# Kernel optimization log

Measured on AMD Instinct MI355X. Metric: run time of the kernel, lower is better.

## Reference

```python
import jax, jax.numpy as jnp
import numpy as np

B, T, F = 16384, 48, 4
UNITS = 256
OUT_STEPS = 24


def setup_inputs() -> dict:
    key = jax.random.key(0)
    ks = jax.random.split(key, 6)
    s_x = 1.0 / np.sqrt(F)
    s_h = 1.0 / np.sqrt(UNITS)
    return {
        "x": jax.random.normal(ks[0], (B, T, F), jnp.float32),
        "Wx": jax.random.normal(ks[1], (F, 4 * UNITS), jnp.float32) * s_x,
        "Wh": jax.random.normal(ks[2], (UNITS, 4 * UNITS), jnp.float32) * s_h,
        "b": jnp.zeros((4 * UNITS,), jnp.float32),
        "Wd": jax.random.normal(ks[3], (UNITS, F), jnp.float32) * s_h,
        "bd": jnp.zeros((F,), jnp.float32),
    }


def _lstm_cell(xt, h, c, Wx, Wh, b):
    # Keras LSTMCell gate order: i, f, g(cell candidate), o
    z = xt @ Wx + h @ Wh + b  # [B, 4*units]
    i, f, g, o = jnp.split(z, 4, axis=-1)
    i = jax.nn.sigmoid(i)
    f = jax.nn.sigmoid(f)
    g = jnp.tanh(g)
    o = jax.nn.sigmoid(o)
    c_new = f * c + i * g
    h_new = o * jnp.tanh(c_new)
    return h_new, c_new


def reference(x, Wx, Wh, b, Wd, bd):
    bsz = x.shape[0]
    h0 = jnp.zeros((bsz, UNITS), x.dtype)
    c0 = jnp.zeros((bsz, UNITS), x.dtype)

    # --- warmup: run LSTM over the input window, keep final state ---
    def warm_step(carry, xt):
        h, c = carry
        h, c = _lstm_cell(xt, h, c, Wx, Wh, b)
        return (h, c), None

    (h, c), _ = jax.lax.scan(warm_step, (h0, c0), jnp.swapaxes(x, 0, 1))
    pred0 = h @ Wd + bd  # first prediction [B, F]

    def ar_step(carry, _):
        h, c, pred = carry
        h, c = _lstm_cell(pred, h, c, Wx, Wh, b)
        pred = h @ Wd + bd
        return (h, c, pred), pred

    _, preds = jax.lax.scan(ar_step, (h, c, pred0), None, length=OUT_STEPS - 1)
    preds = jnp.concatenate([pred0[None], preds], axis=0)  # [out_steps, B, F]
    return jnp.swapaxes(preds, 0, 1)  # [B, out_steps, F]
```

## Files before the change

kernel.cpp:

```cpp
#include <hip/hip_runtime.h>


typedef unsigned short u16;
typedef __attribute__((ext_vector_type(8))) short bf16x8;
typedef __attribute__((ext_vector_type(4))) float f32x4;
typedef __attribute__((ext_vector_type(16))) float f32x16;

#define PITCH 296
#define HB 18944
#define WARM 48
#define STEPS 71
#define LOG2E  1.442695041f
#define LOG2E2 2.885390082f

__device__ __forceinline__ u16 f2bf(float f) {
    unsigned u = __float_as_uint(f);
    u += 0x7FFFu + ((u >> 16) & 1u);
    return (u16)(u >> 16);
}

__device__ __forceinline__ unsigned pk_bf16(float a, float b) {
    unsigned d;
    asm("v_cvt_pk_bf16_f32 %0, %1, %2" : "=v"(d) : "v"(a), "v"(b));
    return d;
}

__device__ __forceinline__ void sync_lds() {
    asm volatile("s_waitcnt lgkmcnt(0)\n\ts_barrier" ::: "memory");
}

__global__ void prep_weights(const float* __restrict__ Wx,
                             const float* __restrict__ Wh,
                             const float* __restrict__ b,
                             const float* __restrict__ Wd,
                             const float* __restrict__ bd,
                             u16* __restrict__ whext,
                             u16* __restrict__ wdp) {
    int idx = blockIdx.x * 256 + threadIdx.x;
    if (idx < 34816) {
        int lane = idx & 63;
        int fr = idx >> 6;
        int g = fr & 3;
        int wv = (fr >> 2) & 7;
        int kt = fr >> 5;
        int k0 = kt * 16 + (lane >> 5) * 8;
        int n = 256 * g + 32 * wv + (lane & 31);
        float sc = (g == 2) ? LOG2E2 : LOG2E;
        u16 v[8];
#pragma unroll
        for (int j = 0; j < 8; ++j) {
            int k = k0 + j;
            float f = 0.0f;
            if (k < 256) f = Wh[k * 1024 + n];
            else if (k < 260) f = Wx[(k - 256) * 1024 + n];
            else if (k == 260) f = b[n];
            v[j] = f2bf(f * sc);
        }
        ushort4* dst = (ushort4*)(whext + (size_t)idx * 8);
        dst[0] = make_ushort4(v[0], v[1], v[2], v[3]);
        dst[1] = make_ushort4(v[4], v[5], v[6], v[7]);
    } else if (idx < 34816 + 576) {
        int id2 = idx - 34816;
        int lane = id2 & 63;
        int kc = id2 >> 6;
        int m = lane & 15;
        int k0 = kc * 32 + (lane >> 4) * 8;
        u16 v[8];
#pragma unroll
        for (int j = 0; j < 8; ++j) {
            int k = k0 + j;
            float f = 0.0f;
            if (m < 4) {
                if (k < 256) f = Wd[k * 4 + m];
                else if (k == 260) f = bd[m];
            }
            v[j] = f2bf(f);
        }
        ushort4* dst = (ushort4*)(wdp + (size_t)id2 * 8);
        dst[0] = make_ushort4(v[0], v[1], v[2], v[3]);
        dst[1] = make_ushort4(v[4], v[5], v[6], v[7]);
    }
}

#define WL(DST, T) do {                                                       \
    const char* _p = wpw + ((size_t)(T) << 15);                               \
    DST[0] = *(const bf16x8*)(_p + voffl);                                    \
    DST[1] = *(const bf16x8*)(_p + voffl + 1024);                             \
    DST[2] = *(const bf16x8*)(_p + voffl + 2048);                             \
    DST[3] = *(const bf16x8*)(_p + voffl + 3072);                             \
} while (0)

#define HL(DST, T) do {                                                       \
    DST[0] = *(const bf16x8*)&hr[hrow0 + (T) * 16];                           \
    DST[1] = *(const bf16x8*)&hr[hrow1 + (T) * 16];                           \
} while (0)

#define MT(WA, HBX)                                                           \
    _Pragma("unroll") for (int m = 0; m < 2; ++m)                             \
    _Pragma("unroll") for (int g = 0; g < 4; ++g)                             \
        acc[m][g] = __builtin_amdgcn_mfma_f32_32x32x16_bf16(                  \
            WA[g], HBX[m], acc[m][g], 0, 0, 0);

#define STG(K, AW, HBX) do { MT(AW, HBX); WL(AW, (K) + 3); HL(HBX, (K) + 2); } while (0)

__global__ __launch_bounds__(512, 2) void lstm_main(
    const float* __restrict__ x, const u16* __restrict__ whext,
    const u16* __restrict__ wdp, float* __restrict__ out) {
    __shared__ __align__(16) u16 hbuf[2 * HB];

    const int tid = threadIdx.x;
    const int w = tid >> 6;
    const int l = tid & 63;
    const int l31 = l & 31;
    const int lh = l >> 5;
    const long long rowBase = (long long)blockIdx.x * 64;

    {
        int4 z = make_int4(0, 0, 0, 0);
        for (int i = tid; i < 4736; i += 512) ((int4*)hbuf)[i] = z;
    }
    sync_lds();
    if (tid < 64) {
        hbuf[tid * PITCH + 260] = (u16)0x3F80;
        hbuf[HB + tid * PITCH + 260] = (u16)0x3F80;
        const float4 xv = *(const float4*)(x + (rowBase + tid) * 192);
        uint2* p = (uint2*)&hbuf[tid * PITCH + 256];
        *p = make_uint2(pk_bf16(xv.x, xv.y), pk_bf16(xv.z, xv.w));
    }

    const char* __restrict__ wpw = (const char*)whext + (size_t)w * 4096;
    const char* __restrict__ dp = (const char*)wdp;
    const int voffl = l * 16;
    const int hrow0 = l31 * PITCH + lh * 8;
    const int hrow1 = (32 + l31) * PITCH + lh * 8;

    f32x16 c[2] = {};
    bf16x8 aw0[4], aw1[4], aw2[4];
    WL(aw0, 0);
    WL(aw1, 1);
    WL(aw2, 2);

    for (int step = 0; step < STEPS; ++step) {
        const u16* hr = hbuf + (step & 1) * HB;
        u16* hw = hbuf + ((step & 1) ^ 1) * HB;

        float4 xv = make_float4(0.f, 0.f, 0.f, 0.f);
        if (w == 0 && step < WARM - 1)
            xv = *(const float4*)(x + (rowBase + l) * 192 + (step + 1) * 4);

        sync_lds();

        f32x16 acc[2][4] = {};
        bf16x8 hb0[2], hb1[2];
        HL(hb0, 0);
        HL(hb1, 1);

        STG(0, aw0, hb0);
        STG(1, aw1, hb1);
#pragma unroll 1
        for (int k = 2; k < 14; k += 6) {
            STG(k + 0, aw2, hb0);
            STG(k + 1, aw0, hb1);
            STG(k + 2, aw1, hb0);
            STG(k + 3, aw2, hb1);
            STG(k + 4, aw0, hb0);
            STG(k + 5, aw1, hb1);
        }
        MT(aw2, hb0); WL(aw2, 2); HL(hb0, 16);
        MT(aw0, hb1); WL(aw0, 0);
        MT(aw1, hb0); WL(aw1, 1);

#pragma unroll
        for (int m = 0; m < 2; ++m) {
            const int hwrow = (32 * m + l31) * PITCH + 32 * w + 4 * lh;
#pragma unroll
            for (int q = 0; q < 4; ++q) {
                unsigned pk[2];
#pragma unroll
                for (int hp = 0; hp < 2; ++hp) {
                    float h2[2];
#pragma unroll
                    for (int rr = 0; rr < 2; ++rr) {
                        const int r = q * 4 + hp * 2 + rr;
                        float ei = __builtin_amdgcn_exp2f(-acc[m][0][r]);
                        float ef = __builtin_amdgcn_exp2f(-acc[m][1][r]);
                        float eg = __builtin_amdgcn_exp2f(-acc[m][2][r]);
                        float eo = __builtin_amdgcn_exp2f(-acc[m][3][r]);
                        float ai = 1.0f + ei, af = 1.0f + ef;
                        float ag = 1.0f + eg, ao = 1.0f + eo;
                        float P  = ai * ag;
                        float rD = __builtin_amdgcn_rcpf(P * af);
                        float cn = fmaf(c[m][r] * P, rD, (1.0f - eg) * af * rD);
                        c[m][r] = cn;
                        float ec = __builtin_amdgcn_exp2f(-LOG2E2 * cn);
                        float rE = __builtin_amdgcn_rcpf(ao * (1.0f + ec));
                        h2[rr] = (1.0f - ec) * rE;
                    }
                    pk[hp] = pk_bf16(h2[0], h2[1]);
                }
                *(uint2*)&hw[hwrow + 8 * q] = make_uint2(pk[0], pk[1]);
            }
        }

        if (step < WARM - 1) {
            if (w == 0) {
                uint2* p = (uint2*)&hw[l * PITCH + 256];
                *p = make_uint2(pk_bf16(xv.x, xv.y), pk_bf16(xv.z, xv.w));
            }
        } else {
            sync_lds();
            if (w < 4) {
                f32x4 pacc = {};
                const int col = l & 15;
                const int prow = (16 * w + col) * PITCH + (l >> 4) * 8;
#pragma unroll
                for (int kc = 0; kc < 9; ++kc) {
                    bf16x8 hbp = *(const bf16x8*)&hw[prow + kc * 32];
                    bf16x8 wap = *(const bf16x8*)(dp + ((size_t)kc * 64 + l) * 16);
                    pacc = __builtin_amdgcn_mfma_f32_16x16x32_bf16(wap, hbp, pacc, 0, 0, 0);
                }
                if ((l >> 4) == 0) {
                    int s = step - (WARM - 1);
                    int batch = 16 * w + col;
                    *(float4*)&out[((rowBase + batch) * 24 + s) * 4] =
                        make_float4(pacc[0], pacc[1], pacc[2], pacc[3]);
                    *(uint2*)&hw[batch * PITCH + 256] =
                        make_uint2(pk_bf16(pacc[0], pacc[1]), pk_bf16(pacc[2], pacc[3]));
                }
            }
        }
    }
}

extern "C" void kernel_launch(void* const* d_in, const int* in_sizes, int n_in,
                              void* d_out, int out_size, void* d_ws, size_t ws_size,
                              hipStream_t stream) {
    const float* x  = (const float*)d_in[0];
    const float* Wx = (const float*)d_in[1];
    const float* Wh = (const float*)d_in[2];
    const float* b  = (const float*)d_in[3];
    const float* Wd = (const float*)d_in[4];
    const float* bd = (const float*)d_in[5];
    float* out = (float*)d_out;

    u16* whext = (u16*)d_ws;
    u16* wdp = (u16*)((char*)d_ws + 557056);

    prep_weights<<<(34816 + 576 + 255) / 256, 256, 0, stream>>>(Wx, Wh, b, Wd, bd, whext, wdp);
    lstm_main<<<256, 512, 0, stream>>>(x, whext, wdp, out);
}
```

Before: 744.3 us.

## Halve rows per block to 32 and double grid with higher occupancy

Each block now handles 32 batch rows instead of 64, so the grid doubles to 512 blocks and launch bounds allow 4 blocks per CU. The MFMA tile drops from two M-subtiles to one, and weight prefetch drops from triple buffering to a single buffer reloaded each stage. This aims to raise occupancy and cut per-thread registers and LDS, so more warps hide latency. In exchange, each weight fragment loaded from global/L2 feeds half as many MFMAs, so total weight traffic per batch row doubles and there is less in-flight prefetch.

```diff
diff --git a/kernel.cpp b/kernel.cpp
--- a/kernel.cpp
+++ b/kernel.cpp
@@ -7,7 +7,7 @@
 typedef __attribute__((ext_vector_type(16))) float f32x16;
 
 #define PITCH 296
-#define HB 18944
+#define HB 9472
 #define WARM 48
 #define STEPS 71
 #define LOG2E  1.442695041f
@@ -90,20 +90,16 @@
     DST[3] = *(const bf16x8*)(_p + voffl + 3072);                             \
 } while (0)
 
-#define HL(DST, T) do {                                                       \
-    DST[0] = *(const bf16x8*)&hr[hrow0 + (T) * 16];                           \
-    DST[1] = *(const bf16x8*)&hr[hrow1 + (T) * 16];                           \
-} while (0)
-
-#define MT(WA, HBX)                                                           \
-    _Pragma("unroll") for (int m = 0; m < 2; ++m)                             \
+#define HL1(DST, T) do { DST = *(const bf16x8*)&hr[hrow + (T) * 16]; } while (0)
+
+#define MT1(HBX)                                                              \
     _Pragma("unroll") for (int g = 0; g < 4; ++g)                             \
-        acc[m][g] = __builtin_amdgcn_mfma_f32_32x32x16_bf16(                  \
-            WA[g], HBX[m], acc[m][g], 0, 0, 0);
-
-#define STG(K, AW, HBX) do { MT(AW, HBX); WL(AW, (K) + 3); HL(HBX, (K) + 2); } while (0)
-
-__global__ __launch_bounds__(512, 2) void lstm_main(
+        acc[g] = __builtin_amdgcn_mfma_f32_32x32x16_bf16(                     \
+            aw[g], HBX, acc[g], 0, 0, 0);
+
+#define STG1(K, HBX) do { MT1(HBX); WL(aw, (K) + 1); HL1(HBX, (K) + 2); } while (0)
+
+__global__ __launch_bounds__(512, 4) void lstm_main(
     const float* __restrict__ x, const u16* __restrict__ whext,
     const u16* __restrict__ wdp, float* __restrict__ out) {
     __shared__ __align__(16) u16 hbuf[2 * HB];
@@ -113,14 +109,14 @@
     const int l = tid & 63;
     const int l31 = l & 31;
     const int lh = l >> 5;
-    const long long rowBase = (long long)blockIdx.x * 64;
+    const long long rowBase = (long long)blockIdx.x * 32;
 
     {
         int4 z = make_int4(0, 0, 0, 0);
-        for (int i = tid; i < 4736; i += 512) ((int4*)hbuf)[i] = z;
+        for (int i = tid; i < 2368; i += 512) ((int4*)hbuf)[i] = z;
     }
     sync_lds();
-    if (tid < 64) {
+    if (tid < 32) {
         hbuf[tid * PITCH + 260] = (u16)0x3F80;
         hbuf[HB + tid * PITCH + 260] = (u16)0x3F80;
         const float4 xv = *(const float4*)(x + (rowBase + tid) * 192);
@@ -131,48 +127,38 @@
     const char* __restrict__ wpw = (const char*)whext + (size_t)w * 4096;
     const char* __restrict__ dp = (const char*)wdp;
     const int voffl = l * 16;
-    const int hrow0 = l31 * PITCH + lh * 8;
-    const int hrow1 = (32 + l31) * PITCH + lh * 8;
-
-    f32x16 c[2] = {};
-    bf16x8 aw0[4], aw1[4], aw2[4];
-    WL(aw0, 0);
-    WL(aw1, 1);
-    WL(aw2, 2);
+    const int hrow = l31 * PITCH + lh * 8;
+
+    f32x16 c = {};
+    bf16x8 aw[4];
+    WL(aw, 0);
 
     for (int step = 0; step < STEPS; ++step) {
         const u16* hr = hbuf + (step & 1) * HB;
         u16* hw = hbuf + ((step & 1) ^ 1) * HB;
 
         float4 xv = make_float4(0.f, 0.f, 0.f, 0.f);
-        if (w == 0 && step < WARM - 1)
+        if (w == 0 && l < 32 && step < WARM - 1)
             xv = *(const float4*)(x + (rowBase + l) * 192 + (step + 1) * 4);
 
         sync_lds();
 
-        f32x16 acc[2][4] = {};
-        bf16x8 hb0[2], hb1[2];
-        HL(hb0, 0);
-        HL(hb1, 1);
-
-        STG(0, aw0, hb0);
-        STG(1, aw1, hb1);
+        f32x16 acc[4] = {};
+        bf16x8 hb0, hb1;
+        HL1(hb0, 0);
+        HL1(hb1, 1);
+
 #pragma unroll 1
-        for (int k = 2; k < 14; k += 6) {
-            STG(k + 0, aw2, hb0);
-            STG(k + 1, aw0, hb1);
-            STG(k + 2, aw1, hb0);
-            STG(k + 3, aw2, hb1);
-            STG(k + 4, aw0, hb0);
-            STG(k + 5, aw1, hb1);
-        }
-        MT(aw2, hb0); WL(aw2, 2); HL(hb0, 16);
-        MT(aw0, hb1); WL(aw0, 0);
-        MT(aw1, hb0); WL(aw1, 1);
-
-#pragma unroll
-        for (int m = 0; m < 2; ++m) {
-            const int hwrow = (32 * m + l31) * PITCH + 32 * w + 4 * lh;
+        for (int k = 0; k < 14; k += 2) {
+            STG1(k, hb0);
+            STG1(k + 1, hb1);
+        }
+        MT1(hb0); WL(aw, 15); HL1(hb0, 16);
+        MT1(hb1); WL(aw, 16);
+        MT1(hb0); WL(aw, 0);
+
+        {
+            const int hwrow = l31 * PITCH + 32 * w + 4 * lh;
 #pragma unroll
             for (int q = 0; q < 4; ++q) {
                 unsigned pk[2];
@@ -182,16 +168,16 @@
 #pragma unroll
                     for (int rr = 0; rr < 2; ++rr) {
                         const int r = q * 4 + hp * 2 + rr;
-                        float ei = __builtin_amdgcn_exp2f(-acc[m][0][r]);
-                        float ef = __builtin_amdgcn_exp2f(-acc[m][1][r]);
-                        float eg = __builtin_amdgcn_exp2f(-acc[m][2][r]);
-                        float eo = __builtin_amdgcn_exp2f(-acc[m][3][r]);
+                        float ei = __builtin_amdgcn_exp2f(-acc[0][r]);
+                        float ef = __builtin_amdgcn_exp2f(-acc[1][r]);
+                        float eg = __builtin_amdgcn_exp2f(-acc[2][r]);
+                        float eo = __builtin_amdgcn_exp2f(-acc[3][r]);
                         float ai = 1.0f + ei, af = 1.0f + ef;
                         float ag = 1.0f + eg, ao = 1.0f + eo;
                         float P  = ai * ag;
                         float rD = __builtin_amdgcn_rcpf(P * af);
-                        float cn = fmaf(c[m][r] * P, rD, (1.0f - eg) * af * rD);
-                        c[m][r] = cn;
+                        float cn = fmaf(c[r] * P, rD, (1.0f - eg) * af * rD);
+                        c[r] = cn;
                         float ec = __builtin_amdgcn_exp2f(-LOG2E2 * cn);
                         float rE = __builtin_amdgcn_rcpf(ao * (1.0f + ec));
                         h2[rr] = (1.0f - ec) * rE;
@@ -203,13 +189,13 @@
         }
 
         if (step < WARM - 1) {
-            if (w == 0) {
+            if (w == 0 && l < 32) {
                 uint2* p = (uint2*)&hw[l * PITCH + 256];
                 *p = make_uint2(pk_bf16(xv.x, xv.y), pk_bf16(xv.z, xv.w));
             }
         } else {
             sync_lds();
-            if (w < 4) {
+            if (w < 2) {
                 f32x4 pacc = {};
                 const int col = l & 15;
                 const int prow = (16 * w + col) * PITCH + (l >> 4) * 8;
@@ -247,5 +233,5 @@
     u16* wdp = (u16*)((char*)d_ws + 557056);
 
     prep_weights<<<(34816 + 576 + 255) / 256, 256, 0, stream>>>(Wx, Wh, b, Wd, bd, whext, wdp);
-    lstm_main<<<256, 512, 0, stream>>>(x, whext, wdp, out);
-}
+    lstm_main<<<512, 512, 0, stream>>>(x, whext, wdp, out);
+}
```

Measured after the change: 924.9 us. 24.3% more time.

## Move LSTM cell state to LDS and deepen weight prefetch pipeline

Applied to the files above, without the earlier changes.

The per-thread cell state (32 floats) moves out of registers into a 64KB LDS buffer and is read and written per quad during the gate epilogue. The freed registers hold two more weight fragment buffers, so weight loads are issued five stages ahead instead of three and the K loop is fully unrolled. The goal is to hide global weight-load latency behind MFMA work. In exchange each step adds LDS traffic for the cell state, and total LDS use per block grows a lot, which may limit occupancy at the requested two blocks per CU.

```diff
diff --git a/kernel.cpp b/kernel.cpp
--- a/kernel.cpp
+++ b/kernel.cpp
@@ -101,12 +101,13 @@
         acc[m][g] = __builtin_amdgcn_mfma_f32_32x32x16_bf16(                  \
             WA[g], HBX[m], acc[m][g], 0, 0, 0);
 
-#define STG(K, AW, HBX) do { MT(AW, HBX); WL(AW, (K) + 3); HL(HBX, (K) + 2); } while (0)
+#define STG(K, AW, HBX) do { MT(AW, HBX); WL(AW, (K) + 5); HL(HBX, (K) + 2); } while (0)
 
 __global__ __launch_bounds__(512, 2) void lstm_main(
     const float* __restrict__ x, const u16* __restrict__ whext,
     const u16* __restrict__ wdp, float* __restrict__ out) {
     __shared__ __align__(16) u16 hbuf[2 * HB];
+    __shared__ __align__(16) float cbuf[16384];
 
     const int tid = threadIdx.x;
     const int w = tid >> 6;
@@ -118,6 +119,7 @@
     {
         int4 z = make_int4(0, 0, 0, 0);
         for (int i = tid; i < 4736; i += 512) ((int4*)hbuf)[i] = z;
+        for (int i = tid; i < 4096; i += 512) ((int4*)cbuf)[i] = z;
     }
     sync_lds();
     if (tid < 64) {
@@ -134,11 +136,12 @@
     const int hrow0 = l31 * PITCH + lh * 8;
     const int hrow1 = (32 + l31) * PITCH + lh * 8;
 
-    f32x16 c[2] = {};
-    bf16x8 aw0[4], aw1[4], aw2[4];
+    bf16x8 aw0[4], aw1[4], aw2[4], aw3[4], aw4[4];
     WL(aw0, 0);
     WL(aw1, 1);
     WL(aw2, 2);
+    WL(aw3, 3);
+    WL(aw4, 4);
 
     for (int step = 0; step < STEPS; ++step) {
         const u16* hr = hbuf + (step & 1) * HB;
@@ -157,16 +160,19 @@
 
         STG(0, aw0, hb0);
         STG(1, aw1, hb1);
-#pragma unroll 1
-        for (int k = 2; k < 14; k += 6) {
-            STG(k + 0, aw2, hb0);
-            STG(k + 1, aw0, hb1);
-            STG(k + 2, aw1, hb0);
-            STG(k + 3, aw2, hb1);
-            STG(k + 4, aw0, hb0);
-            STG(k + 5, aw1, hb1);
-        }
-        MT(aw2, hb0); WL(aw2, 2); HL(hb0, 16);
+        STG(2, aw2, hb0);
+        STG(3, aw3, hb1);
+        STG(4, aw4, hb0);
+        STG(5, aw0, hb1);
+        STG(6, aw1, hb0);
+        STG(7, aw2, hb1);
+        STG(8, aw3, hb0);
+        STG(9, aw4, hb1);
+        STG(10, aw0, hb0);
+        STG(11, aw1, hb1);
+        MT(aw2, hb0); WL(aw2, 2); HL(hb0, 14);
+        MT(aw3, hb1); WL(aw3, 3); HL(hb1, 15);
+        MT(aw4, hb0); WL(aw4, 4); HL(hb0, 16);
         MT(aw0, hb1); WL(aw0, 0);
         MT(aw1, hb0); WL(aw1, 1);
 
@@ -175,6 +181,9 @@
             const int hwrow = (32 * m + l31) * PITCH + 32 * w + 4 * lh;
 #pragma unroll
             for (int q = 0; q < 4; ++q) {
+                float* cp = cbuf + ((m * 4 + q) << 11) + (tid << 2);
+                f32x4 cv = *(const f32x4*)cp;
+                f32x4 nv;
                 unsigned pk[2];
 #pragma unroll
                 for (int hp = 0; hp < 2; ++hp) {
@@ -182,6 +191,7 @@
 #pragma unroll
                     for (int rr = 0; rr < 2; ++rr) {
                         const int r = q * 4 + hp * 2 + rr;
+                        const int rc = hp * 2 + rr;
                         float ei = __builtin_amdgcn_exp2f(-acc[m][0][r]);
                         float ef = __builtin_amdgcn_exp2f(-acc[m][1][r]);
                         float eg = __builtin_amdgcn_exp2f(-acc[m][2][r]);
@@ -190,14 +200,15 @@
                         float ag = 1.0f + eg, ao = 1.0f + eo;
                         float P  = ai * ag;
                         float rD = __builtin_amdgcn_rcpf(P * af);
-                        float cn = fmaf(c[m][r] * P, rD, (1.0f - eg) * af * rD);
-                        c[m][r] = cn;
+                        float cn = fmaf(cv[rc] * P, rD, (1.0f - eg) * af * rD);
+                        nv[rc] = cn;
                         float ec = __builtin_amdgcn_exp2f(-LOG2E2 * cn);
                         float rE = __builtin_amdgcn_rcpf(ao * (1.0f + ec));
                         h2[rr] = (1.0f - ec) * rE;
                     }
                     pk[hp] = pk_bf16(h2[0], h2[1]);
                 }
+                *(f32x4*)cp = nv;
                 *(uint2*)&hw[hwrow + 8 * q] = make_uint2(pk[0], pk[1]);
             }
         }
```

Measured after the change: 788.8 us. 6.0% more time.

## Replace per-step block barriers with LDS flag-based producer/consumer sync and triple buffering

Applied to the files above, without the earlier changes.

Removes the workgroup-wide s_barrier at each recurrent step. Each wave now publishes a per-wave LDS flag after writing its slice of h, and consumers spin only on the flags of the h k-tiles they need. The h buffer grows from double to triple buffering so fast waves can run ahead without overwriting data still being read. Each wave also starts its k-loop at a different tile offset, so it can begin on its own freshly written tiles. The cost is spin-polling on volatile LDS loads, more LDS use that may affect occupancy, and a risk of subtle ordering bugs.

```diff
diff --git a/kernel.cpp b/kernel.cpp
--- a/kernel.cpp
+++ b/kernel.cpp
@@ -25,8 +25,25 @@
     return d;
 }
 
-__device__ __forceinline__ void sync_lds() {
-    asm volatile("s_waitcnt lgkmcnt(0)\n\ts_barrier" ::: "memory");
+__device__ __forceinline__ void set_flag(int* f, int v, int lane) {
+    asm volatile("s_waitcnt lgkmcnt(0)" ::: "memory");
+    if (lane == 0) *(volatile int*)f = v;
+}
+
+__device__ __forceinline__ void wait1(const int* f, int tgt) {
+    while (*(volatile const int*)f < tgt) {}
+    asm volatile("" ::: "memory");
+}
+
+__device__ __forceinline__ void wait4(const int* f, int tgt) {
+    for (;;) {
+        int a = ((volatile const int*)f)[0];
+        int b = ((volatile const int*)f)[1];
+        int c = ((volatile const int*)f)[2];
+        int d = ((volatile const int*)f)[3];
+        if (a >= tgt && b >= tgt && c >= tgt && d >= tgt) break;
+    }
+    asm volatile("" ::: "memory");
 }
 
 __global__ void prep_weights(const float* __restrict__ Wx,
@@ -82,17 +99,17 @@
     }
 }
 
-#define WL(DST, T) do {                                                       \
-    const char* _p = wpw + ((size_t)(T) << 15);                               \
+#define WLK(DST, KT) do {                                                     \
+    const char* _p = wpw + ((size_t)(KT) << 15);                              \
     DST[0] = *(const bf16x8*)(_p + voffl);                                    \
     DST[1] = *(const bf16x8*)(_p + voffl + 1024);                             \
     DST[2] = *(const bf16x8*)(_p + voffl + 2048);                             \
     DST[3] = *(const bf16x8*)(_p + voffl + 3072);                             \
 } while (0)
 
-#define HL(DST, T) do {                                                       \
-    DST[0] = *(const bf16x8*)&hr[hrow0 + (T) * 16];                           \
-    DST[1] = *(const bf16x8*)&hr[hrow1 + (T) * 16];                           \
+#define HLD(DST, KT) do {                                                     \
+    DST[0] = *(const bf16x8*)&hr[hrow0 + (KT) * 16];                          \
+    DST[1] = *(const bf16x8*)&hr[hrow1 + (KT) * 16];                          \
 } while (0)
 
 #define MT(WA, HBX)                                                           \
@@ -101,12 +118,12 @@
         acc[m][g] = __builtin_amdgcn_mfma_f32_32x32x16_bf16(                  \
             WA[g], HBX[m], acc[m][g], 0, 0, 0);
 
-#define STG(K, AW, HBX) do { MT(AW, HBX); WL(AW, (K) + 3); HL(HBX, (K) + 2); } while (0)
-
 __global__ __launch_bounds__(512, 2) void lstm_main(
     const float* __restrict__ x, const u16* __restrict__ whext,
     const u16* __restrict__ wdp, float* __restrict__ out) {
-    __shared__ __align__(16) u16 hbuf[2 * HB];
+    __shared__ __align__(16) u16 hbuf[3 * HB];
+    __shared__ int flagH[8];
+    __shared__ int flag16[4];
 
     const int tid = threadIdx.x;
     const int w = tid >> 6;
@@ -117,16 +134,20 @@
 
     {
         int4 z = make_int4(0, 0, 0, 0);
-        for (int i = tid; i < 4736; i += 512) ((int4*)hbuf)[i] = z;
-    }
-    sync_lds();
+        for (int i = tid; i < 7104; i += 512) ((int4*)hbuf)[i] = z;
+        if (tid < 8) flagH[tid] = 0;
+        if (tid < 4) flag16[tid] = 0;
+    }
+    __syncthreads();
     if (tid < 64) {
         hbuf[tid * PITCH + 260] = (u16)0x3F80;
         hbuf[HB + tid * PITCH + 260] = (u16)0x3F80;
+        hbuf[2 * HB + tid * PITCH + 260] = (u16)0x3F80;
         const float4 xv = *(const float4*)(x + (rowBase + tid) * 192);
         uint2* p = (uint2*)&hbuf[tid * PITCH + 256];
         *p = make_uint2(pk_bf16(xv.x, xv.y), pk_bf16(xv.z, xv.w));
     }
+    __syncthreads();
 
     const char* __restrict__ wpw = (const char*)whext + (size_t)w * 4096;
     const char* __restrict__ dp = (const char*)wdp;
@@ -135,40 +156,46 @@
     const int hrow1 = (32 + l31) * PITCH + lh * 8;
 
     f32x16 c[2] = {};
-    bf16x8 aw0[4], aw1[4], aw2[4];
-    WL(aw0, 0);
-    WL(aw1, 1);
-    WL(aw2, 2);
-
+    bf16x8 aw[3][4];
+    bf16x8 hb[2][2];
+    WLK(aw[0], 2 * w);
+    WLK(aw[1], 2 * w + 1);
+    WLK(aw[2], (2 * w + 2) & 15);
+
+    int rb = 0;
     for (int step = 0; step < STEPS; ++step) {
-        const u16* hr = hbuf + (step & 1) * HB;
-        u16* hw = hbuf + ((step & 1) ^ 1) * HB;
+        int wb = rb + 1; if (wb == 3) wb = 0;
+        const u16* hr = hbuf + rb * HB;
+        u16* hw = hbuf + wb * HB;
 
         float4 xv = make_float4(0.f, 0.f, 0.f, 0.f);
         if (w == 0 && step < WARM - 1)
             xv = *(const float4*)(x + (rowBase + l) * 192 + (step + 1) * 4);
 
-        sync_lds();
-
         f32x16 acc[2][4] = {};
-        bf16x8 hb0[2], hb1[2];
-        HL(hb0, 0);
-        HL(hb1, 1);
-
-        STG(0, aw0, hb0);
-        STG(1, aw1, hb1);
-#pragma unroll 1
-        for (int k = 2; k < 14; k += 6) {
-            STG(k + 0, aw2, hb0);
-            STG(k + 1, aw0, hb1);
-            STG(k + 2, aw1, hb0);
-            STG(k + 3, aw2, hb1);
-            STG(k + 4, aw0, hb0);
-            STG(k + 5, aw1, hb1);
-        }
-        MT(aw2, hb0); WL(aw2, 2); HL(hb0, 16);
-        MT(aw0, hb1); WL(aw0, 0);
-        MT(aw1, hb0); WL(aw1, 1);
+        HLD(hb[0], 2 * w);
+        HLD(hb[1], 2 * w + 1);
+
+#pragma unroll
+        for (int j = 0; j < 17; ++j) {
+            MT(aw[j % 3], hb[j & 1]);
+            if (j <= 14) {
+                const int t2 = j + 2;
+                if (t2 == 16) {
+                    wait4(flag16, step);
+                    HLD(hb[j & 1], 16);
+                } else {
+                    if ((t2 & 1) == 0)
+                        wait1(&flagH[(w + t2 / 2) & 7], step);
+                    HLD(hb[j & 1], (2 * w + t2) & 15);
+                }
+            }
+            {
+                const int tt = (j <= 13) ? (j + 3) : ((j - 12) % 3);
+                const int kt3 = (tt < 16) ? ((2 * w + tt) & 15) : 16;
+                WLK(aw[j % 3], kt3);
+            }
+        }
 
 #pragma unroll
         for (int m = 0; m < 2; ++m) {
@@ -201,34 +228,38 @@
                 *(uint2*)&hw[hwrow + 8 * q] = make_uint2(pk[0], pk[1]);
             }
         }
+        set_flag(&flagH[w], step + 1, l);
 
         if (step < WARM - 1) {
             if (w == 0) {
                 uint2* p = (uint2*)&hw[l * PITCH + 256];
                 *p = make_uint2(pk_bf16(xv.x, xv.y), pk_bf16(xv.z, xv.w));
-            }
-        } else {
-            sync_lds();
-            if (w < 4) {
-                f32x4 pacc = {};
-                const int col = l & 15;
-                const int prow = (16 * w + col) * PITCH + (l >> 4) * 8;
-#pragma unroll
-                for (int kc = 0; kc < 9; ++kc) {
-                    bf16x8 hbp = *(const bf16x8*)&hw[prow + kc * 32];
-                    bf16x8 wap = *(const bf16x8*)(dp + ((size_t)kc * 64 + l) * 16);
-                    pacc = __builtin_amdgcn_mfma_f32_16x16x32_bf16(wap, hbp, pacc, 0, 0, 0);
-                }
-                if ((l >> 4) == 0) {
-                    int s = step - (WARM - 1);
-                    int batch = 16 * w + col;
-                    *(float4*)&out[((rowBase + batch) * 24 + s) * 4] =
-                        make_float4(pacc[0], pacc[1], pacc[2], pacc[3]);
-                    *(uint2*)&hw[batch * PITCH + 256] =
-                        make_uint2(pk_bf16(pacc[0], pacc[1]), pk_bf16(pacc[2], pacc[3]));
-                }
-            }
-        }
+                asm volatile("s_waitcnt lgkmcnt(0)" ::: "memory");
+                if (l < 4) *(volatile int*)&flag16[l] = step + 1;
+            }
+        } else if (w < 4) {
+            wait4(flagH, step + 1);
+            wait4(flagH + 4, step + 1);
+            f32x4 pacc = {};
+            const int col = l & 15;
+            const int prow = (16 * w + col) * PITCH + (l >> 4) * 8;
+#pragma unroll
+            for (int kc = 0; kc < 9; ++kc) {
+                bf16x8 hbp = *(const bf16x8*)&hw[prow + kc * 32];
+                bf16x8 wap = *(const bf16x8*)(dp + ((size_t)kc * 64 + l) * 16);
+                pacc = __builtin_amdgcn_mfma_f32_16x16x32_bf16(wap, hbp, pacc, 0, 0, 0);
+            }
+            if ((l >> 4) == 0) {
+                int s = step - (WARM - 1);
+                int batch = 16 * w + col;
+                *(float4*)&out[((rowBase + batch) * 24 + s) * 4] =
+                    make_float4(pacc[0], pacc[1], pacc[2], pacc[3]);
+                *(uint2*)&hw[batch * PITCH + 256] =
+                    make_uint2(pk_bf16(pacc[0], pacc[1]), pk_bf16(pacc[2], pacc[3]));
+            }
+            set_flag(&flag16[w], step + 1, l);
+        }
+        rb = wb;
     }
 }
 
```

Result: slower. 1.377 ms (+85.0%).
